# Kernel optimization log

Hardware: AMD Instinct MI355X
Metric: run time of the kernel (lower is better)

## Reference

```python
import jax, jax.numpy as jnp
import numpy as np

B, S, N_STATE, N_HEAD = 2, 2048, 1024, 16
HEAD_DIM = N_STATE // N_HEAD


def setup_inputs() -> dict:
    key = jax.random.key(0)
    ks = jax.random.split(key, 9)
    w_scale = N_STATE ** -0.5
    x = jax.random.normal(ks[0], (B, S, N_STATE), jnp.float32)
    # Whisper-style additive causal mask with -inf above the diagonal
    mask = jnp.triu(jnp.full((S, S), -jnp.inf, jnp.float32), k=1)
    Wq = jax.random.normal(ks[1], (N_STATE, N_STATE), jnp.float32) * w_scale
    bq = jax.random.normal(ks[2], (N_STATE,), jnp.float32) * 0.01
    Wk = jax.random.normal(ks[3], (N_STATE, N_STATE), jnp.float32) * w_scale  # no bias
    Wv = jax.random.normal(ks[4], (N_STATE, N_STATE), jnp.float32) * w_scale
    bv = jax.random.normal(ks[5], (N_STATE,), jnp.float32) * 0.01
    Wo = jax.random.normal(ks[6], (N_STATE, N_STATE), jnp.float32) * w_scale
    bo = jax.random.normal(ks[7], (N_STATE,), jnp.float32) * 0.01
    return {"x": x, "mask": mask, "Wq": Wq, "bq": bq, "Wk": Wk,
            "Wv": Wv, "bv": bv, "Wo": Wo, "bo": bo}


def reference(x, mask, Wq, bq, Wk, Wv, bv, Wo, bo):
    b, s, n_state = x.shape
    scale = (n_state // N_HEAD) ** -0.25
    q = (x @ Wq + bq).reshape(b, s, N_HEAD, HEAD_DIM)  # [b,s,h,d]
    k = (x @ Wk).reshape(b, s, N_HEAD, HEAD_DIM)
    v = (x @ Wv + bv).reshape(b, s, N_HEAD, HEAD_DIM)
    # scale applied to both q and k as in source
    qk = jnp.einsum('bqhd,bkhd->bhqk', q * scale, k * scale)
    qk = qk + mask[:s, :s]
    qk = qk.astype(jnp.float32)
    qk = jnp.where(jnp.isinf(qk), -1e9, qk)
    w = jax.nn.softmax(qk, axis=-1).astype(q.dtype)  # [b,h,q,k]
    wv = jnp.einsum('bhqk,bkhd->bqhd', w, v).reshape(b, s, n_state)
    out = wv @ Wo + bo
    return (out, qk)
```

## Files before the change

### kernel.cpp

```cpp
#include <hip/hip_runtime.h>

typedef __attribute__((ext_vector_type(8))) short short8;
typedef __attribute__((ext_vector_type(4))) float f32x4;

#define SEQ   2048
#define NST   1024
#define NHD   16
#define HDM   64
#define BSZ   2
#define MTOT  (BSZ*SEQ)

__device__ __forceinline__ unsigned short f2bf(float f) {
    union { float f; unsigned int u; } v; v.f = f;
    return (unsigned short)((v.u + 0x7fffu + ((v.u >> 16) & 1u)) >> 16);
}

__device__ __forceinline__ void gload_lds16(const void* g, void* l) {
    __builtin_amdgcn_global_load_lds((const __attribute__((address_space(1))) void*)g,
                                     (__attribute__((address_space(3))) void*)l, 16, 0, 0);
}

__global__ void k_convert(const float* __restrict__ x, unsigned short* __restrict__ out, int n) {
    int i = (blockIdx.x * 256 + threadIdx.x) * 8;
    if (i >= n) return;
    float4 a = *(const float4*)(x + i);
    float4 b = *(const float4*)(x + i + 4);
    short8 v;
    v[0] = (short)f2bf(a.x); v[1] = (short)f2bf(a.y);
    v[2] = (short)f2bf(a.z); v[3] = (short)f2bf(a.w);
    v[4] = (short)f2bf(b.x); v[5] = (short)f2bf(b.y);
    v[6] = (short)f2bf(b.z); v[7] = (short)f2bf(b.w);
    *(short8*)(out + i) = v;
}

__global__ void k_transpose4(const float* __restrict__ W0, const float* __restrict__ W1,
                             const float* __restrict__ W2, const float* __restrict__ W3,
                             unsigned short* __restrict__ Wt) {
    __shared__ float t[32][33];
    const float* W = (blockIdx.z == 0) ? W0 : (blockIdx.z == 1) ? W1 : (blockIdx.z == 2) ? W2 : W3;
    unsigned short* dst = Wt + ((size_t)blockIdx.z << 20);
    int n0 = blockIdx.x * 32, k0 = blockIdx.y * 32;
    int c = threadIdx.x & 31, rr = threadIdx.x >> 5;
    for (int i = 0; i < 4; i++) {
        int r = i * 8 + rr;
        t[r][c] = W[(k0 + r) * NST + n0 + c];
    }
    __syncthreads();
    for (int i = 0; i < 4; i++) {
        int r = i * 8 + rr;
        dst[(n0 + r) * NST + k0 + c] = f2bf(t[c][r]);
    }
}

__global__ void k_vt(const unsigned short* __restrict__ v, unsigned short* __restrict__ vt) {
    __shared__ unsigned short t[64 * 72];
    int jt = blockIdx.x, bh = blockIdx.y;
    int b = bh >> 4, h = bh & 15;
    int tid = threadIdx.x;
    for (int i = 0; i < 2; i++) {
        int id = i * 256 + tid;
        int row = id >> 3, dc = (id & 7) * 8;
        *(short8*)(t + row * 72 + dc) =
            *(const short8*)(v + ((size_t)(b * SEQ + jt * 64 + row)) * NST + h * HDM + dc);
    }
    __syncthreads();
    for (int i = 0; i < 2; i++) {
        int id = i * 256 + tid;
        int d = id >> 3, jc = (id & 7) * 8;
        short8 vv;
        for (int u = 0; u < 8; u++) vv[u] = (short)t[(jc + u) * 72 + d];
        *(short8*)(vt + ((size_t)(bh * HDM + d)) * SEQ + jt * 64 + jc) = vv;
    }
}

template<int MODE>
__global__ __launch_bounds__(256) void k_gemm128(const unsigned short* __restrict__ A,
                                                 const unsigned short* __restrict__ Bt,
                                                 const float* __restrict__ bias0,
                                                 const float* __restrict__ bias2,
                                                 float scale, void* __restrict__ outp) {
    constexpr int BN = (MODE == 1) ? 128 : 64;
    constexpr int NI = BN / 32;
    __shared__ __align__(16) unsigned short As[128 * 64];
    __shared__ __align__(16) unsigned short Bs[BN * 64];
    int m0 = blockIdx.y * 128, n0 = blockIdx.x * BN;
    int tid = threadIdx.x, lane = tid & 63, wave = tid >> 6;
    int quad = lane >> 4, l16 = lane & 15;
    int wm = (wave & 1) * 64, wn = (wave >> 1) * (BN / 2);
    int srow = lane >> 3, spb = lane & 7;
    f32x4 acc[4][NI] = {};
    for (int k0 = 0; k0 < NST; k0 += 64) {
        __syncthreads();
        for (int j = 0; j < 4; j++) {
            int row = wave * 32 + j * 8 + srow;
            int blk = (spb ^ (row & 7)) * 8;
            gload_lds16(A + (size_t)(m0 + row) * NST + k0 + blk, As + (wave * 32 + j * 8) * 64);
        }
        for (int j = 0; j < NI; j++) {
            int row = wave * (8 * NI) + j * 8 + srow;
            int blk = (spb ^ (row & 7)) * 8;
            gload_lds16(Bt + (size_t)(n0 + row) * NST + k0 + blk, Bs + (wave * 8 * NI + j * 8) * 64);
        }
        __syncthreads();
        for (int ks = 0; ks < 2; ks++) {
            short8 a[4], b[NI];
            for (int mi = 0; mi < 4; mi++) {
                int r = wm + mi * 16 + l16;
                a[mi] = *(const short8*)(As + r * 64 + (((ks * 4 + quad) ^ (r & 7)) * 8));
            }
            for (int ni = 0; ni < NI; ni++) {
                int r = wn + ni * 16 + l16;
                b[ni] = *(const short8*)(Bs + r * 64 + (((ks * 4 + quad) ^ (r & 7)) * 8));
            }
            for (int mi = 0; mi < 4; mi++)
                for (int ni = 0; ni < NI; ni++)
                    acc[mi][ni] = __builtin_amdgcn_mfma_f32_16x16x32_bf16(a[mi], b[ni], acc[mi][ni], 0, 0, 0);
        }
    }
    for (int ni = 0; ni < NI; ni++) {
        int ncol = n0 + wn + ni * 16 + l16;
        if (MODE == 1) {
            int mat = ncol >> 10, c = ncol & 1023;
            float bs = (mat == 0) ? bias0[c] : (mat == 2 ? bias2[c] : 0.0f);
            float sc = (mat == 2) ? 1.0f : scale;
            unsigned short* dst = (unsigned short*)outp + ((size_t)mat << 22) + c;
            for (int mi = 0; mi < 4; mi++)
                for (int r = 0; r < 4; r++) {
                    int row = m0 + wm + mi * 16 + quad * 4 + r;
                    dst[(size_t)row * NST] = f2bf((acc[mi][ni][r] + bs) * sc);
                }
        } else {
            float bs = bias0[ncol];
            for (int mi = 0; mi < 4; mi++)
                for (int r = 0; r < 4; r++) {
                    int row = m0 + wm + mi * 16 + quad * 4 + r;
                    ((float*)outp)[(size_t)row * NST + ncol] = acc[mi][ni][r] + bs;
                }
        }
    }
}

__global__ __launch_bounds__(256) void k_attn(const unsigned short* __restrict__ qb,
                                              const unsigned short* __restrict__ kb,
                                              const unsigned short* __restrict__ vtg,
                                              float* __restrict__ qk,
                                              unsigned short* __restrict__ wv) {
    __shared__ __align__(16) unsigned short Ks[2][64 * 64];
    __shared__ __align__(16) unsigned short Vs[2][64 * 64];
    __shared__ __align__(16) unsigned short Plds[4 * 16 * 72];
    int pair = blockIdx.x, bh = blockIdx.y;
    int b = bh >> 4, h = bh & 15;
    int tid = threadIdx.x, lane = tid & 63, wave = tid >> 6;
    int quad = lane >> 4, l16 = lane & 15;
    unsigned short* pbuf = Plds + wave * 16 * 72;
    int srow = lane >> 3;
    int spb = lane & 7;
    short o1 = (short)0x3F80;
    short8 vones = {o1, o1, o1, o1, o1, o1, o1, o1};
    int fx0 = (quad ^ (l16 & 7)) * 8;
    int fx1 = ((quad + 4) ^ (l16 & 7)) * 8;
    int cur = 0;

    for (int phase = 0; phase < 2; ++phase) {
        int qt = phase ? (31 - pair) : pair;
        int qrow = qt * 64 + wave * 16;
        const unsigned short* qp = qb + ((size_t)(b * SEQ + qrow + l16)) * NST + h * HDM + quad * 8;
        short8 aq0 = *(const short8*)qp;
        short8 aq1 = *(const short8*)(qp + 32);
        f32x4 o[4] = {};
        f32x4 lac = {};

        __syncthreads();
        for (int j = 0; j < 2; j++) {
            int row = wave * 16 + j * 8 + srow;
            int lb = (spb ^ (row & 7)) * 8;
            gload_lds16(kb + ((size_t)(b * SEQ + row)) * NST + h * HDM + lb,
                        Ks[cur] + (wave * 16 + j * 8) * 64);
            gload_lds16(vtg + ((size_t)(bh * HDM + row)) * SEQ + lb,
                        Vs[cur] + (wave * 16 + j * 8) * 64);
        }

        for (int jt = 0; jt <= qt; jt++) {
            int j0 = jt * 64;
            __syncthreads();
            if (jt < qt) {
                int jn = j0 + 64;
                for (int j = 0; j < 2; j++) {
                    int row = wave * 16 + j * 8 + srow;
                    int lb = (spb ^ (row & 7)) * 8;
                    gload_lds16(kb + ((size_t)(b * SEQ + jn + row)) * NST + h * HDM + lb,
                                Ks[cur ^ 1] + (wave * 16 + j * 8) * 64);
                    gload_lds16(vtg + ((size_t)(bh * HDM + row)) * SEQ + jn + lb,
                                Vs[cur ^ 1] + (wave * 16 + j * 8) * 64);
                }
            }
            const unsigned short* KsC = Ks[cur];
            const unsigned short* VsC = Vs[cur];

            f32x4 s[4];
            for (int c = 0; c < 4; c++) {
                int base = (c * 16 + l16) * 64;
                short8 b0 = *(const short8*)(KsC + base + fx0);
                short8 b1 = *(const short8*)(KsC + base + fx1);
                f32x4 z = {};
                z = __builtin_amdgcn_mfma_f32_16x16x32_bf16(aq0, b0, z, 0, 0, 0);
                s[c] = __builtin_amdgcn_mfma_f32_16x16x32_bf16(aq1, b1, z, 0, 0, 0);
            }

            bool diag = (jt == qt);
            for (int r = 0; r < 4; r++) {
                int i_g = qrow + quad * 4 + r;
                float* qrow_ptr = qk + ((size_t)bh * SEQ + i_g) * SEQ + j0;
                for (int c = 0; c < 4; c++) {
                    int jc = c * 16 + l16;
                    float val = s[c][r];
                    if (diag && (j0 + jc > i_g)) val = -1e9f;
                    __builtin_nontemporal_store(val, qrow_ptr + jc);
                    float pe = __expf(val - 16.0f);
                    pbuf[(quad * 4 + r) * 72 + jc] = f2bf(pe);
                }
            }
            short8 ap0 = *(const short8*)(pbuf + l16 * 72 + quad * 8);
            short8 ap1 = *(const short8*)(pbuf + l16 * 72 + 32 + quad * 8);
            for (int db = 0; db < 4; db++) {
                int base = (db * 16 + l16) * 64;
                short8 b0 = *(const short8*)(VsC + base + fx0);
                short8 b1 = *(const short8*)(VsC + base + fx1);
                o[db] = __builtin_amdgcn_mfma_f32_16x16x32_bf16(ap0, b0, o[db], 0, 0, 0);
                o[db] = __builtin_amdgcn_mfma_f32_16x16x32_bf16(ap1, b1, o[db], 0, 0, 0);
            }
            lac = __builtin_amdgcn_mfma_f32_16x16x32_bf16(ap0, vones, lac, 0, 0, 0);
            lac = __builtin_amdgcn_mfma_f32_16x16x32_bf16(ap1, vones, lac, 0, 0, 0);
            cur ^= 1;
        }

        for (int db = 0; db < 4; db++) {
            for (int r = 0; r < 4; r++) {
                int row = qrow + quad * 4 + r;
                wv[((size_t)(b * SEQ + row)) * NST + h * HDM + db * 16 + l16] = f2bf(o[db][r] / lac[r]);
            }
        }

        f32x4 neg = {-1e9f, -1e9f, -1e9f, -1e9f};
        int c0 = (qt + 1) * 64;
        for (int r = 0; r < 16; r++) {
            float* rp = qk + ((size_t)bh * SEQ + qrow + r) * SEQ;
            for (int c = c0 + lane * 4; c < SEQ; c += 256)
                __builtin_nontemporal_store(neg, (f32x4*)(rp + c));
        }
    }
}

extern "C" void kernel_launch(void* const* d_in, const int* in_sizes, int n_in,
                              void* d_out, int out_size, void* d_ws, size_t ws_size,
                              hipStream_t stream) {
    (void)in_sizes; (void)n_in; (void)out_size; (void)ws_size;
    const float* x  = (const float*)d_in[0];
    const float* Wq = (const float*)d_in[2];
    const float* bq = (const float*)d_in[3];
    const float* Wk = (const float*)d_in[4];
    const float* Wv = (const float*)d_in[5];
    const float* bv = (const float*)d_in[6];
    const float* Wo = (const float*)d_in[7];
    const float* bo = (const float*)d_in[8];

    float* out_f  = (float*)d_out;
    float* qk_out = out_f + (size_t)MTOT * NST;

    unsigned short* ws = (unsigned short*)d_ws;
    unsigned short* xb   = ws;
    unsigned short* wqt  = ws + (size_t)4 * 1024 * 1024;
    unsigned short* wot  = ws + (size_t)7 * 1024 * 1024;
    unsigned short* qbuf = ws + (size_t)8  * 1024 * 1024;
    unsigned short* kbuf = ws + (size_t)12 * 1024 * 1024;
    unsigned short* vbuf = ws + (size_t)16 * 1024 * 1024;
    unsigned short* vtb  = ws + (size_t)20 * 1024 * 1024;
    unsigned short* wvb  = xb;

    const float scale = 0.3535533905932738f;

    k_convert<<<2048, 256, 0, stream>>>(x, xb, MTOT * NST);
    k_transpose4<<<dim3(32, 32, 4), 256, 0, stream>>>(Wq, Wk, Wv, Wo, wqt);

    k_gemm128<1><<<dim3(24, 32), 256, 0, stream>>>(xb, wqt, bq, bv, scale, qbuf);

    k_vt<<<dim3(32, 32), 256, 0, stream>>>(vbuf, vtb);
    k_attn<<<dim3(16, 32), 256, 0, stream>>>(qbuf, kbuf, vtb, qk_out, wvb);

    k_gemm128<0><<<dim3(16, 32), 256, 0, stream>>>(wvb, wot, bo, nullptr, 1.0f, (void*)out_f);
}
```

Measured before the change: 721.6 us.

## Merge convert and transpose kernels, remap attention blocks, add MFMA priority hints

Folds the fp32-to-bf16 conversion of x into the weight transpose kernel as an extra grid slice, which removes one kernel launch. The attention kernel gets a new block-index mapping that spreads batch-heads across consecutive blocks, meant to improve load balance and cache locality. It also wraps the MFMA sections in s_setprio hints and splits the exp/bf16 write into its own loop after the qk stores. Each change is small, and the priority and reorder effects depend on how the compiler schedules the code.

Measured after the change: 697.9 us. 3.3% less time.

```diff
diff --git a/kernel.cpp b/kernel.cpp
--- a/kernel.cpp
+++ b/kernel.cpp
@@ -20,22 +20,25 @@
                                      (__attribute__((address_space(3))) void*)l, 16, 0, 0);
 }
 
-__global__ void k_convert(const float* __restrict__ x, unsigned short* __restrict__ out, int n) {
-    int i = (blockIdx.x * 256 + threadIdx.x) * 8;
-    if (i >= n) return;
-    float4 a = *(const float4*)(x + i);
-    float4 b = *(const float4*)(x + i + 4);
-    short8 v;
-    v[0] = (short)f2bf(a.x); v[1] = (short)f2bf(a.y);
-    v[2] = (short)f2bf(a.z); v[3] = (short)f2bf(a.w);
-    v[4] = (short)f2bf(b.x); v[5] = (short)f2bf(b.y);
-    v[6] = (short)f2bf(b.z); v[7] = (short)f2bf(b.w);
-    *(short8*)(out + i) = v;
-}
-
-__global__ void k_transpose4(const float* __restrict__ W0, const float* __restrict__ W1,
-                             const float* __restrict__ W2, const float* __restrict__ W3,
-                             unsigned short* __restrict__ Wt) {
+__global__ void k_prep(const float* __restrict__ W0, const float* __restrict__ W1,
+                       const float* __restrict__ W2, const float* __restrict__ W3,
+                       unsigned short* __restrict__ Wt,
+                       const float* __restrict__ x, unsigned short* __restrict__ xb) {
+    if (blockIdx.z == 4) {
+        int bid = blockIdx.x + 32 * blockIdx.y;
+        size_t i = ((size_t)bid * 256 + threadIdx.x) * 16;
+        for (int half = 0; half < 2; half++) {
+            float4 a = *(const float4*)(x + i + half * 8);
+            float4 b = *(const float4*)(x + i + half * 8 + 4);
+            short8 v;
+            v[0] = (short)f2bf(a.x); v[1] = (short)f2bf(a.y);
+            v[2] = (short)f2bf(a.z); v[3] = (short)f2bf(a.w);
+            v[4] = (short)f2bf(b.x); v[5] = (short)f2bf(b.y);
+            v[6] = (short)f2bf(b.z); v[7] = (short)f2bf(b.w);
+            *(short8*)(xb + i + half * 8) = v;
+        }
+        return;
+    }
     __shared__ float t[32][33];
     const float* W = (blockIdx.z == 0) ? W0 : (blockIdx.z == 1) ? W1 : (blockIdx.z == 2) ? W2 : W3;
     unsigned short* dst = Wt + ((size_t)blockIdx.z << 20);
@@ -148,7 +151,9 @@
     __shared__ __align__(16) unsigned short Ks[2][64 * 64];
     __shared__ __align__(16) unsigned short Vs[2][64 * 64];
     __shared__ __align__(16) unsigned short Plds[4 * 16 * 72];
-    int pair = blockIdx.x, bh = blockIdx.y;
+    int n = blockIdx.x + 16 * blockIdx.y;
+    int bh = (n & 7) + 8 * ((n >> 3) & 3);
+    int pair = n >> 5;
     int b = bh >> 4, h = bh & 15;
     int tid = threadIdx.x, lane = tid & 63, wave = tid >> 6;
     int quad = lane >> 4, l16 = lane & 15;
@@ -198,6 +203,7 @@
             const unsigned short* VsC = Vs[cur];
 
             f32x4 s[4];
+            __builtin_amdgcn_s_setprio(1);
             for (int c = 0; c < 4; c++) {
                 int base = (c * 16 + l16) * 64;
                 short8 b0 = *(const short8*)(KsC + base + fx0);
@@ -206,8 +212,10 @@
                 z = __builtin_amdgcn_mfma_f32_16x16x32_bf16(aq0, b0, z, 0, 0, 0);
                 s[c] = __builtin_amdgcn_mfma_f32_16x16x32_bf16(aq1, b1, z, 0, 0, 0);
             }
+            __builtin_amdgcn_s_setprio(0);
 
             bool diag = (jt == qt);
+            float pv[4][4];
             for (int r = 0; r < 4; r++) {
                 int i_g = qrow + quad * 4 + r;
                 float* qrow_ptr = qk + ((size_t)bh * SEQ + i_g) * SEQ + j0;
@@ -216,12 +224,16 @@
                     float val = s[c][r];
                     if (diag && (j0 + jc > i_g)) val = -1e9f;
                     __builtin_nontemporal_store(val, qrow_ptr + jc);
-                    float pe = __expf(val - 16.0f);
-                    pbuf[(quad * 4 + r) * 72 + jc] = f2bf(pe);
+                    pv[r][c] = val;
                 }
             }
+            for (int r = 0; r < 4; r++)
+                for (int c = 0; c < 4; c++)
+                    pbuf[(quad * 4 + r) * 72 + c * 16 + l16] = f2bf(__expf(pv[r][c] - 16.0f));
+
             short8 ap0 = *(const short8*)(pbuf + l16 * 72 + quad * 8);
             short8 ap1 = *(const short8*)(pbuf + l16 * 72 + 32 + quad * 8);
+            __builtin_amdgcn_s_setprio(1);
             for (int db = 0; db < 4; db++) {
                 int base = (db * 16 + l16) * 64;
                 short8 b0 = *(const short8*)(VsC + base + fx0);
@@ -231,6 +243,7 @@
             }
             lac = __builtin_amdgcn_mfma_f32_16x16x32_bf16(ap0, vones, lac, 0, 0, 0);
             lac = __builtin_amdgcn_mfma_f32_16x16x32_bf16(ap1, vones, lac, 0, 0, 0);
+            __builtin_amdgcn_s_setprio(0);
             cur ^= 1;
         }
 
@@ -279,8 +292,7 @@
 
     const float scale = 0.3535533905932738f;
 
-    k_convert<<<2048, 256, 0, stream>>>(x, xb, MTOT * NST);
-    k_transpose4<<<dim3(32, 32, 4), 256, 0, stream>>>(Wq, Wk, Wv, Wo, wqt);
+    k_prep<<<dim3(32, 32, 5), 256, 0, stream>>>(Wq, Wk, Wv, Wo, wqt, x, xb);
 
     k_gemm128<1><<<dim3(24, 32), 256, 0, stream>>>(xb, wqt, bq, bv, scale, qbuf);
 
```
